# Optimization experiments

Hardware: AMD Instinct MI355X
Metric: run time of the kernel (lower is better)

Reference implementation:

```python
import jax, jax.numpy as jnp
import numpy as np

H = 16  # num_heads


def setup_inputs() -> dict:
    key = jax.random.key(0)
    ks = jax.random.split(key, 8)
    B, T, D = 2, 2048, 1024
    hd = D // H
    s = 0.02
    return {
        "x": jax.random.normal(ks[0], (B, T, D), jnp.float32),
        "position_bias": jax.random.normal(ks[1], (H, T, T), jnp.float32) * 0.1,
        "Wq": jax.random.normal(ks[2], (D, D), jnp.float32) * s,
        "bq": jnp.zeros((D,), jnp.float32),
        "Wk": jax.random.normal(ks[3], (D, D), jnp.float32) * s,
        "bk": jnp.zeros((D,), jnp.float32),
        "Wv": jax.random.normal(ks[4], (D, D), jnp.float32) * s,
        "bv": jnp.zeros((D,), jnp.float32),
        "Wo": jax.random.normal(ks[5], (D, D), jnp.float32) * s,
        "bo": jnp.zeros((D,), jnp.float32),
        "Wg": jax.random.normal(ks[6], (8, hd), jnp.float32) * s,
        "bg": jnp.zeros((8,), jnp.float32),
        "gru_const": jnp.ones((1, H, 1, 1), jnp.float32),
    }


def reference(x, position_bias, Wq, bq, Wk, bk, Wv, bv, Wo, bo, Wg, bg, gru_const):
    B, T, D = x.shape
    hd = D // H
    # gated relative position bias
    gated_input = x.reshape(B, T, H, hd).transpose(0, 2, 1, 3)  # (B,H,T,hd)
    rp = jnp.einsum('bhtd,ed->bhte', gated_input, Wg) + bg       # (B,H,T,8)
    rp = rp.reshape(B, H, T, 2, 4).sum(-1)                        # (B,H,T,2)
    rp = jax.nn.sigmoid(rp)
    gate_a, gate_b = rp[..., 0:1], rp[..., 1:2]                   # (B,H,T,1)
    gate_input = gate_a * (gate_b * gru_const - 1.0) + 2.0        # (B,H,T,1)
    gated_bias = gate_input * position_bias                       # (B,H,T,T)
    # scaled dot-product attention
    q = (x @ Wq.T + bq).reshape(B, T, H, hd).transpose(0, 2, 1, 3)
    k = (x @ Wk.T + bk).reshape(B, T, H, hd).transpose(0, 2, 1, 3)
    v = (x @ Wv.T + bv).reshape(B, T, H, hd).transpose(0, 2, 1, 3)
    scale = 1.0 / jnp.sqrt(jnp.asarray(hd, x.dtype))
    scores = jnp.einsum('bhqd,bhkd->bhqk', q, k) * scale + gated_bias
    attn = jax.nn.softmax(scores, axis=-1)
    out = jnp.einsum('bhqk,bhkd->bhqd', attn, v)                  # (B,H,T,hd)
    out = out.transpose(0, 2, 1, 3).reshape(B, T, D)
    return out @ Wo.T + bo
```

## Files before the change

kernel.cpp:

```cpp
#include <hip/hip_runtime.h>
#include <stdint.h>

typedef unsigned short u16;
typedef __attribute__((ext_vector_type(8))) short short8;
typedef __attribute__((ext_vector_type(4))) float f32x4;

__device__ __forceinline__ u16 f2bf(float f) {
  union { float f; uint32_t u; } v; v.f = f;
  uint32_t r = (v.u + 0x7fffu + ((v.u >> 16) & 1u)) >> 16;
  return (u16)r;
}

__device__ __forceinline__ f32x4 mfma16(short8 a, short8 b, f32x4 c) {
  return __builtin_amdgcn_mfma_f32_16x16x32_bf16(a, b, c, 0, 0, 0);
}

typedef __attribute__((address_space(3))) void lds_void;
typedef __attribute__((address_space(1))) void glb_void;
__device__ __forceinline__ void gld_lds16(const void* gp, void* lp) {
  __builtin_amdgcn_global_load_lds((const glb_void*)gp, (lds_void*)lp, 16, 0, 0);
}

__global__ __launch_bounds__(256) void cvt_bf16(const float* __restrict__ in,
                                                u16* __restrict__ out, int n4) {
  int i = blockIdx.x * 256 + threadIdx.x;
  if (i >= n4) return;
  const float4 v = ((const float4*)in)[i];
  ushort4 o;
  o.x = f2bf(v.x); o.y = f2bf(v.y); o.z = f2bf(v.z); o.w = f2bf(v.w);
  ((ushort4*)out)[i] = o;
}

__global__ __launch_bounds__(256) void gates_kernel(
    const float* __restrict__ x, const float* __restrict__ Wg,
    const float* __restrict__ bg, const float* __restrict__ gru,
    float* __restrict__ gates) {
  __shared__ float wga[64], wgb[64], bsum[2];
  int tid = threadIdx.x;
  if (tid < 64) {
    float a = 0.f, b = 0.f;
#pragma unroll
    for (int e = 0; e < 4; ++e) a += Wg[e * 64 + tid];
#pragma unroll
    for (int e = 4; e < 8; ++e) b += Wg[e * 64 + tid];
    wga[tid] = a; wgb[tid] = b;
  }
  if (tid == 0) bsum[0] = bg[0] + bg[1] + bg[2] + bg[3];
  if (tid == 1) bsum[1] = bg[4] + bg[5] + bg[6] + bg[7];
  __syncthreads();
  int l16 = tid & 15;
  int row = blockIdx.x * 16 + (tid >> 4);
  int b = row >> 15, h = (row >> 11) & 15, t = row & 2047;
  const float4 xv = *(const float4*)&x[(b * 2048 + t) * 1024 + h * 64 + l16 * 4];
  float pa = xv.x * wga[l16 * 4] + xv.y * wga[l16 * 4 + 1] +
             xv.z * wga[l16 * 4 + 2] + xv.w * wga[l16 * 4 + 3];
  float pq = xv.x * wgb[l16 * 4] + xv.y * wgb[l16 * 4 + 1] +
             xv.z * wgb[l16 * 4 + 2] + xv.w * wgb[l16 * 4 + 3];
#pragma unroll
  for (int off = 1; off < 16; off <<= 1) {
    pa += __shfl_xor(pa, off);
    pq += __shfl_xor(pq, off);
  }
  if (l16 == 0) {
    float ga = 1.f / (1.f + __expf(-(pa + bsum[0])));
    float gb = 1.f / (1.f + __expf(-(pq + bsum[1])));
    gates[row] = ga * (gb * gru[h] - 1.0f) + 2.0f;
  }
}

__global__ __launch_bounds__(256) void gemm_bt(
    const u16* __restrict__ A,
    const u16* __restrict__ W0, const u16* __restrict__ W1, const u16* __restrict__ W2,
    const float* __restrict__ c0, const float* __restrict__ c1, const float* __restrict__ c2,
    void* d0, void* d1, void* d2, int fbase) {
  __shared__ __align__(16) u16 As[128 * 32];
  __shared__ __align__(16) u16 Bs[128 * 32];
  const int z = blockIdx.z;
  const int f = fbase + z;
  const u16* W = (z == 0) ? W0 : (z == 1 ? W1 : W2);
  const float* bias = (z == 0) ? c0 : (z == 1 ? c1 : c2);
  void* dst = (z == 0) ? d0 : (z == 1 ? d1 : d2);

  const int m0 = blockIdx.x * 128, n0 = blockIdx.y * 128;
  const int tid = threadIdx.x;
  const int w = tid >> 6, lane = tid & 63, l16 = lane & 15, quad = lane >> 4;
  const int wm = w >> 1, wn = w & 1;

  f32x4 acc[4][4] = {};

  for (int kt = 0; kt < 32; ++kt) {
    const int k0 = kt * 32;
    __syncthreads();
#pragma unroll
    for (int j = 0; j < 2; ++j) {
      int c = tid + j * 256;
      int row = c >> 2, dc = c & 3;
      gld_lds16(&A[(m0 + row) * 1024 + k0 + dc * 8], &As[c * 8]);
      gld_lds16(&W[(n0 + row) * 1024 + k0 + dc * 8], &Bs[c * 8]);
    }
    __syncthreads();
    short8 af[4], bf[4];
#pragma unroll
    for (int i = 0; i < 4; ++i) {
      af[i] = *(const short8*)&As[(wm * 64 + i * 16 + l16) * 32 + quad * 8];
      bf[i] = *(const short8*)&Bs[(wn * 64 + i * 16 + l16) * 32 + quad * 8];
    }
#pragma unroll
    for (int mb = 0; mb < 4; ++mb)
#pragma unroll
      for (int nb = 0; nb < 4; ++nb)
        acc[mb][nb] = mfma16(af[mb], bf[nb], acc[mb][nb]);
  }

  if (f < 3) {
    u16* out = (u16*)dst;
#pragma unroll
    for (int nb = 0; nb < 4; ++nb) {
      int gn = n0 + wn * 64 + nb * 16 + l16;
      float bv = bias[gn];
      int hh = gn >> 6, dd = gn & 63;
#pragma unroll
      for (int mb = 0; mb < 4; ++mb)
#pragma unroll
        for (int r = 0; r < 4; ++r) {
          int gm = m0 + wm * 64 + mb * 16 + quad * 4 + r;
          int bb = gm >> 11, t = gm & 2047;
          out[((bb * 16 + hh) * 2048 + t) * 64 + dd] = f2bf(acc[mb][nb][r] + bv);
        }
    }
  } else {
    float* out = (float*)dst;
#pragma unroll
    for (int nb = 0; nb < 4; ++nb) {
      int gn = n0 + wn * 64 + nb * 16 + l16;
      float bv = bias[gn];
#pragma unroll
      for (int mb = 0; mb < 4; ++mb)
#pragma unroll
        for (int r = 0; r < 4; ++r) {
          int gm = m0 + wm * 64 + mb * 16 + quad * 4 + r;
          out[gm * 1024 + gn] = acc[mb][nb][r] + bv;
        }
    }
  }
}

__global__ __launch_bounds__(256) void vtrans(const u16* __restrict__ v,
                                              u16* __restrict__ vt) {
  __shared__ __align__(16) u16 lds[64 * 72];
  const int bh = blockIdx.y, t0 = blockIdx.x * 64;
  const int tid = threadIdx.x;
#pragma unroll
  for (int j = 0; j < 2; ++j) {
    int c = tid + j * 256;
    int tr = c >> 3, dc = c & 7;
    union { int4 v4; u16 u[8]; } uu;
    uu.v4 = *(const int4*)&v[(bh * 2048 + t0 + tr) * 64 + dc * 8];
#pragma unroll
    for (int jj = 0; jj < 8; ++jj) lds[(dc * 8 + jj) * 72 + tr] = uu.u[jj];
  }
  __syncthreads();
#pragma unroll
  for (int j = 0; j < 2; ++j) {
    int c = tid + j * 256;
    int dr = c >> 3, tc = c & 7;
    int4 vv = *(const int4*)&lds[dr * 72 + tc * 8];
    *(int4*)&vt[(bh * 64 + dr) * 2048 + t0 + tc * 8] = vv;
  }
}

__global__ __launch_bounds__(256) void attn_kernel(
    const u16* __restrict__ q, const u16* __restrict__ k,
    const u16* __restrict__ vt, const float* __restrict__ pb,
    const float* __restrict__ gates, u16* __restrict__ ao) {
  __shared__ __align__(16) u16 Ks[2][64 * 72];
  __shared__ __align__(16) u16 Vs[2][64 * 72];
  __shared__ __align__(16) u16 Ps[4][16 * 72];

  const int qt = blockIdx.x, h = blockIdx.y;
  const int tid = threadIdx.x, w = tid >> 6, lane = tid & 63;
  const int l16 = lane & 15, quad = lane >> 4;
  const int m0 = qt * 64 + w * 16;

  short8 Qa[2][2];
  float g8[2][4];
#pragma unroll
  for (int b = 0; b < 2; ++b) {
    const u16* qp = &q[((b * 16 + h) * 2048 + m0 + l16) * 64];
    Qa[b][0] = *(const short8*)&qp[quad * 8];
    Qa[b][1] = *(const short8*)&qp[32 + quad * 8];
#pragma unroll
    for (int r = 0; r < 4; ++r)
      g8[b][r] = gates[(b * 16 + h) * 2048 + m0 + quad * 4 + r] * 8.0f;
  }

  f32x4 O[2][4] = {};
  float mi[2][4], li[2][4];
#pragma unroll
  for (int b = 0; b < 2; ++b)
#pragma unroll
    for (int r = 0; r < 4; ++r) { mi[b][r] = -3.0e38f; li[b][r] = 0.f; }

  for (int kt = 0; kt < 32; ++kt) {
    const int k0 = kt * 64;
    float pbv[4][4];
#pragma unroll
    for (int nb = 0; nb < 4; ++nb)
#pragma unroll
      for (int r = 0; r < 4; ++r)
        pbv[nb][r] = pb[(h * 2048 + m0 + quad * 4 + r) * 2048 + k0 + nb * 16 + l16];

    __syncthreads();
#pragma unroll
    for (int j = 0; j < 4; ++j) {
      int c = tid + j * 256;
      int bb = c >> 9, row = (c >> 3) & 63, ch = c & 7;
      int4 kv = *(const int4*)&k[((bb * 16 + h) * 2048 + k0 + row) * 64 + ch * 8];
      *(int4*)&Ks[bb][row * 72 + ch * 8] = kv;
      int4 vv = *(const int4*)&vt[((bb * 16 + h) * 64 + row) * 2048 + k0 + ch * 8];
      *(int4*)&Vs[bb][row * 72 + ch * 8] = vv;
    }
    __syncthreads();

#pragma unroll
    for (int b = 0; b < 2; ++b) {
      f32x4 acc[4];
#pragma unroll
      for (int nb = 0; nb < 4; ++nb) {
        short8 kf0 = *(const short8*)&Ks[b][(nb * 16 + l16) * 72 + quad * 8];
        short8 kf1 = *(const short8*)&Ks[b][(nb * 16 + l16) * 72 + 32 + quad * 8];
        f32x4 z = {};
        z = mfma16(Qa[b][0], kf0, z);
        acc[nb] = mfma16(Qa[b][1], kf1, z);
      }
      float Sv[4][4], rm[4];
#pragma unroll
      for (int nb = 0; nb < 4; ++nb)
#pragma unroll
        for (int r = 0; r < 4; ++r)
          Sv[nb][r] = (acc[nb][r] + g8[b][r] * pbv[nb][r]) * 0.125f;
#pragma unroll
      for (int r = 0; r < 4; ++r)
        rm[r] = fmaxf(fmaxf(Sv[0][r], Sv[1][r]), fmaxf(Sv[2][r], Sv[3][r]));
#pragma unroll
      for (int off = 1; off < 16; off <<= 1)
#pragma unroll
        for (int r = 0; r < 4; ++r)
          rm[r] = fmaxf(rm[r], __shfl_xor(rm[r], off));
      float al[4], rs[4];
#pragma unroll
      for (int r = 0; r < 4; ++r) {
        float mn = fmaxf(mi[b][r], rm[r]);
        al[r] = __expf(mi[b][r] - mn);
        mi[b][r] = mn;
        rs[r] = 0.f;
      }
#pragma unroll
      for (int nb = 0; nb < 4; ++nb)
#pragma unroll
        for (int r = 0; r < 4; ++r) {
          float p = __expf(Sv[nb][r] - mi[b][r]);
          Sv[nb][r] = p;
          rs[r] += p;
        }
#pragma unroll
      for (int off = 1; off < 16; off <<= 1)
#pragma unroll
        for (int r = 0; r < 4; ++r)
          rs[r] += __shfl_xor(rs[r], off);
#pragma unroll
      for (int r = 0; r < 4; ++r)
        li[b][r] = li[b][r] * al[r] + rs[r];
#pragma unroll
      for (int hb = 0; hb < 4; ++hb)
#pragma unroll
        for (int r = 0; r < 4; ++r)
          O[b][hb][r] *= al[r];
#pragma unroll
      for (int nb = 0; nb < 4; ++nb)
#pragma unroll
        for (int r = 0; r < 4; ++r)
          Ps[w][(quad * 4 + r) * 72 + nb * 16 + l16] = f2bf(Sv[nb][r]);
      __asm__ volatile("s_waitcnt lgkmcnt(0)" ::: "memory");
      short8 pa0 = *(const short8*)&Ps[w][l16 * 72 + quad * 8];
      short8 pa1 = *(const short8*)&Ps[w][l16 * 72 + 32 + quad * 8];
#pragma unroll
      for (int hb = 0; hb < 4; ++hb) {
        short8 vf0 = *(const short8*)&Vs[b][(hb * 16 + l16) * 72 + quad * 8];
        short8 vf1 = *(const short8*)&Vs[b][(hb * 16 + l16) * 72 + 32 + quad * 8];
        O[b][hb] = mfma16(pa0, vf0, O[b][hb]);
        O[b][hb] = mfma16(pa1, vf1, O[b][hb]);
      }
    }
  }
#pragma unroll
  for (int b = 0; b < 2; ++b) {
    float inv[4];
#pragma unroll
    for (int r = 0; r < 4; ++r) inv[r] = 1.0f / li[b][r];
#pragma unroll
    for (int hb = 0; hb < 4; ++hb)
#pragma unroll
      for (int r = 0; r < 4; ++r) {
        int t = m0 + quad * 4 + r;
        int col = h * 64 + hb * 16 + l16;
        ao[(b * 2048 + t) * 1024 + col] = f2bf(O[b][hb][r] * inv[r]);
      }
  }
}

extern "C" void kernel_launch(void* const* d_in, const int* in_sizes, int n_in,
                              void* d_out, int out_size, void* d_ws, size_t ws_size,
                              hipStream_t stream) {
  const float* x   = (const float*)d_in[0];
  const float* pb  = (const float*)d_in[1];
  const float* Wq  = (const float*)d_in[2];
  const float* bq  = (const float*)d_in[3];
  const float* Wk  = (const float*)d_in[4];
  const float* bk  = (const float*)d_in[5];
  const float* Wv  = (const float*)d_in[6];
  const float* bv  = (const float*)d_in[7];
  const float* Wo  = (const float*)d_in[8];
  const float* bo  = (const float*)d_in[9];
  const float* Wg  = (const float*)d_in[10];
  const float* bg  = (const float*)d_in[11];
  const float* gru = (const float*)d_in[12];
  float* out = (float*)d_out;

  char* ws = (char*)d_ws;
  u16*   xb   = (u16*)(ws);
  u16*   wqb  = (u16*)(ws + (8u  << 20));
  u16*   wkb  = (u16*)(ws + (10u << 20));
  u16*   wvb  = (u16*)(ws + (12u << 20));
  u16*   wob  = (u16*)(ws + (14u << 20));
  u16*   qws  = (u16*)(ws + (16u << 20));
  u16*   kws  = (u16*)(ws + (24u << 20));
  u16*   vws  = (u16*)(ws + (32u << 20));
  u16*   vtws = (u16*)(ws + (40u << 20));
  float* gws  = (float*)(ws + (48u << 20));
  u16*   aows = (u16*)(ws + (49u << 20));

  cvt_bf16<<<4096, 256, 0, stream>>>(x,  xb,  1048576);
  cvt_bf16<<<1024, 256, 0, stream>>>(Wq, wqb, 262144);
  cvt_bf16<<<1024, 256, 0, stream>>>(Wk, wkb, 262144);
  cvt_bf16<<<1024, 256, 0, stream>>>(Wv, wvb, 262144);
  cvt_bf16<<<1024, 256, 0, stream>>>(Wo, wob, 262144);
  gates_kernel<<<4096, 256, 0, stream>>>(x, Wg, bg, gru, gws);
  gemm_bt<<<dim3(32, 8, 3), 256, 0, stream>>>(xb, wqb, wkb, wvb, bq, bk, bv,
                                              qws, kws, vws, 0);
  vtrans<<<dim3(32, 32), 256, 0, stream>>>(vws, vtws);
  attn_kernel<<<dim3(32, 16), 256, 0, stream>>>(qws, kws, vtws, pb, gws, aows);
  gemm_bt<<<dim3(32, 8, 1), 256, 0, stream>>>(aows, wob, wob, wob, bo, bo, bo,
                                              out, out, out, 3);
}
```

Baseline: 556.4 us.

## Load K/V fragments directly from global memory and fuse bf16 conversion launches

The attention kernel no longer stages K and V tiles through shared memory. Each wave loads its MFMA fragments straight from global memory into registers, which removes two block-wide barriers per key tile and the LDS round trip. The cost is that every wave redundantly fetches the same K/V data, relying on cache hits, with higher register pressure, and a launch_bounds occupancy hint of 2 is added. The five fp32-to-bf16 conversion launches are also merged into one kernel to cut launch overhead.

```diff
diff --git a/kernel.cpp b/kernel.cpp
--- a/kernel.cpp
+++ b/kernel.cpp
@@ -21,14 +21,26 @@
   __builtin_amdgcn_global_load_lds((const glb_void*)gp, (lds_void*)lp, 16, 0, 0);
 }
 
-__global__ __launch_bounds__(256) void cvt_bf16(const float* __restrict__ in,
-                                                u16* __restrict__ out, int n4) {
-  int i = blockIdx.x * 256 + threadIdx.x;
-  if (i >= n4) return;
-  const float4 v = ((const float4*)in)[i];
+__global__ __launch_bounds__(256) void cvt_all(
+    const float* __restrict__ x, const float* __restrict__ wq,
+    const float* __restrict__ wk, const float* __restrict__ wv,
+    const float* __restrict__ wo, u16* __restrict__ xb, u16* __restrict__ wqb,
+    u16* __restrict__ wkb, u16* __restrict__ wvb, u16* __restrict__ wob) {
+  int bid = blockIdx.x;
+  const float* src; u16* dst; int base;
+  if (bid < 4096) {
+    src = x; dst = xb; base = bid;
+  } else {
+    int s = (bid - 4096) >> 10, r = (bid - 4096) & 1023;
+    base = r;
+    src = (s == 0) ? wq : (s == 1) ? wk : (s == 2) ? wv : wo;
+    dst = (s == 0) ? wqb : (s == 1) ? wkb : (s == 2) ? wvb : wob;
+  }
+  int i = base * 256 + threadIdx.x;
+  const float4 v = ((const float4*)src)[i];
   ushort4 o;
   o.x = f2bf(v.x); o.y = f2bf(v.y); o.z = f2bf(v.z); o.w = f2bf(v.w);
-  ((ushort4*)out)[i] = o;
+  ((ushort4*)dst)[i] = o;
 }
 
 __global__ __launch_bounds__(256) void gates_kernel(
@@ -169,12 +181,10 @@
   }
 }
 
-__global__ __launch_bounds__(256) void attn_kernel(
+__global__ __launch_bounds__(256, 2) void attn_kernel(
     const u16* __restrict__ q, const u16* __restrict__ k,
     const u16* __restrict__ vt, const float* __restrict__ pb,
     const float* __restrict__ gates, u16* __restrict__ ao) {
-  __shared__ __align__(16) u16 Ks[2][64 * 72];
-  __shared__ __align__(16) u16 Vs[2][64 * 72];
   __shared__ __align__(16) u16 Ps[4][16 * 72];
 
   const int qt = blockIdx.x, h = blockIdx.y;
@@ -210,28 +220,31 @@
       for (int r = 0; r < 4; ++r)
         pbv[nb][r] = pb[(h * 2048 + m0 + quad * 4 + r) * 2048 + k0 + nb * 16 + l16];
 
-    __syncthreads();
-#pragma unroll
-    for (int j = 0; j < 4; ++j) {
-      int c = tid + j * 256;
-      int bb = c >> 9, row = (c >> 3) & 63, ch = c & 7;
-      int4 kv = *(const int4*)&k[((bb * 16 + h) * 2048 + k0 + row) * 64 + ch * 8];
-      *(int4*)&Ks[bb][row * 72 + ch * 8] = kv;
-      int4 vv = *(const int4*)&vt[((bb * 16 + h) * 64 + row) * 2048 + k0 + ch * 8];
-      *(int4*)&Vs[bb][row * 72 + ch * 8] = vv;
-    }
-    __syncthreads();
+    short8 kf[2][4][2];
+#pragma unroll
+    for (int b = 0; b < 2; ++b)
+#pragma unroll
+      for (int nb = 0; nb < 4; ++nb) {
+        const u16* kp = &k[((b * 16 + h) * 2048 + k0 + nb * 16 + l16) * 64];
+        kf[b][nb][0] = *(const short8*)&kp[quad * 8];
+        kf[b][nb][1] = *(const short8*)&kp[32 + quad * 8];
+      }
 
 #pragma unroll
     for (int b = 0; b < 2; ++b) {
+      short8 vf[4][2];
+#pragma unroll
+      for (int hb = 0; hb < 4; ++hb) {
+        const u16* vp = &vt[((b * 16 + h) * 64 + hb * 16 + l16) * 2048 + k0];
+        vf[hb][0] = *(const short8*)&vp[quad * 8];
+        vf[hb][1] = *(const short8*)&vp[32 + quad * 8];
+      }
       f32x4 acc[4];
 #pragma unroll
       for (int nb = 0; nb < 4; ++nb) {
-        short8 kf0 = *(const short8*)&Ks[b][(nb * 16 + l16) * 72 + quad * 8];
-        short8 kf1 = *(const short8*)&Ks[b][(nb * 16 + l16) * 72 + 32 + quad * 8];
         f32x4 z = {};
-        z = mfma16(Qa[b][0], kf0, z);
-        acc[nb] = mfma16(Qa[b][1], kf1, z);
+        z = mfma16(Qa[b][0], kf[b][nb][0], z);
+        acc[nb] = mfma16(Qa[b][1], kf[b][nb][1], z);
       }
       float Sv[4][4], rm[4];
 #pragma unroll
@@ -286,10 +299,8 @@
       short8 pa1 = *(const short8*)&Ps[w][l16 * 72 + 32 + quad * 8];
 #pragma unroll
       for (int hb = 0; hb < 4; ++hb) {
-        short8 vf0 = *(const short8*)&Vs[b][(hb * 16 + l16) * 72 + quad * 8];
-        short8 vf1 = *(const short8*)&Vs[b][(hb * 16 + l16) * 72 + 32 + quad * 8];
-        O[b][hb] = mfma16(pa0, vf0, O[b][hb]);
-        O[b][hb] = mfma16(pa1, vf1, O[b][hb]);
+        O[b][hb] = mfma16(pa0, vf[hb][0], O[b][hb]);
+        O[b][hb] = mfma16(pa1, vf[hb][1], O[b][hb]);
       }
     }
   }
@@ -340,11 +351,7 @@
   float* gws  = (float*)(ws + (48u << 20));
   u16*   aows = (u16*)(ws + (49u << 20));
 
-  cvt_bf16<<<4096, 256, 0, stream>>>(x,  xb,  1048576);
-  cvt_bf16<<<1024, 256, 0, stream>>>(Wq, wqb, 262144);
-  cvt_bf16<<<1024, 256, 0, stream>>>(Wk, wkb, 262144);
-  cvt_bf16<<<1024, 256, 0, stream>>>(Wv, wvb, 262144);
-  cvt_bf16<<<1024, 256, 0, stream>>>(Wo, wob, 262144);
+  cvt_all<<<8192, 256, 0, stream>>>(x, Wq, Wk, Wv, Wo, xb, wqb, wkb, wvb, wob);
   gates_kernel<<<4096, 256, 0, stream>>>(x, Wg, bg, gru, gws);
   gemm_bt<<<dim3(32, 8, 3), 256, 0, stream>>>(xb, wqb, wkb, wvb, bq, bk, bv,
                                               qws, kws, vws, 0);
```

Measured after the change: 660.2 us. 1.19x slower.
